# Optimization experiments

Hardware: AMD Instinct MI355X
Metric: run time of the kernel (lower is better)

The kernel has to match this reference:

```python
import jax, jax.numpy as jnp
import numpy as np


def setup_inputs() -> dict:
    key = jax.random.key(0)
    k1, k2 = jax.random.split(key)
    B, N, M = 8, 8192, 8192
    points1 = jax.random.normal(k1, (B, N, 2), dtype=jnp.float32)
    points2 = jax.random.normal(k2, (B, M, 2), dtype=jnp.float32)
    return {"points1": points1, "points2": points2}


def reference(points1, points2):
    # points1: [B, N, 2], points2: [B, M, 2]
    # Squared pairwise distances via |a|^2 + |b|^2 - 2 a.b  -> [B, N, M]
    p1_sq = jnp.sum(points1 * points1, axis=-1)  # [B, N]
    p2_sq = jnp.sum(points2 * points2, axis=-1)  # [B, M]
    cross = jnp.einsum("bnd,bmd->bnm", points1, points2)  # [B, N, M]
    sqdist = p1_sq[:, :, None] + p2_sq[:, None, :] - 2.0 * cross
    dist1 = jnp.min(sqdist, axis=2)  # [B, N]: NN of each p1 point in p2
    dist2 = jnp.min(sqdist, axis=1)  # [B, M]: NN of each p2 point in p1
    cost = jnp.mean(dist1, axis=-1) + jnp.mean(dist2, axis=-1)  # [B]
    return jnp.sum(cost)
```

## Files before the change

kernel.cpp:

```cpp
#include <hip/hip_runtime.h>


#define BATCH 8
#define NPTS  8192
#define TPB   256
#define IPT   16
#define PPB   (TPB * IPT)
#define TILES (NPTS / PPB)
#define S     32
#define JCH   (NPTS / S)
#define PARTN (2 * BATCH * S * NPTS)

__device__ inline float min3f(float a, float b, float c) {
    float d;
    asm("v_min3_f32 %0, %1, %2, %3" : "=v"(d) : "v"(a), "v"(b), "v"(c));
    return d;
}

__device__ inline float2 pkfma(float2 a, float2 b, float2 c) {
    float2 d;
    asm("v_pk_fma_f32 %0, %1, %2, %3" : "=v"(d) : "v"(a), "v"(b), "v"(c));
    return d;
}

__global__ __launch_bounds__(TPB, 4)
void chamfer_partial(const float* __restrict__ p1, const float* __restrict__ p2,
                     float* __restrict__ partial ) {
    __shared__ __align__(16) float qx[JCH];
    __shared__ __align__(16) float qy[JCH];
    __shared__ __align__(16) float qz[JCH];

    int blk   = blockIdx.x;
    int split = blk & (S - 1);      blk >>= 5;
    int tile  = blk & (TILES - 1);  blk >>= 1;
    int b     = blk & (BATCH - 1);  blk >>= 3;
    int dir   = blk;

    const float2* a  = (const float2*)(dir ? p2 : p1) + (size_t)b * NPTS;
    const float2* bp = (const float2*)(dir ? p1 : p2) + (size_t)b * NPTS + split * JCH;

    int t = threadIdx.x;

    {
        float2 v = bp[t];
        qx[t] = v.x;
        qy[t] = v.y;
        qz[t] = fmaf(v.x, v.x, v.y * v.y);
    }

    int pt_base = tile * PPB;
    float2 xp2[IPT], yp2[IPT];
    float  m[IPT];
#pragma unroll
    for (int k = 0; k < IPT; ++k) {
        float2 v = a[pt_base + k * TPB + t];
        xp2[k] = make_float2(-2.0f * v.x, -2.0f * v.x);
        yp2[k] = make_float2(-2.0f * v.y, -2.0f * v.y);
        m[k]   = 3.0e38f;
    }

    __syncthreads();

    for (int j = 0; j < JCH; j += 8) {
        float4 x03 = *(const float4*)&qx[j];
        float4 x47 = *(const float4*)&qx[j + 4];
        float4 y03 = *(const float4*)&qy[j];
        float4 y47 = *(const float4*)&qy[j + 4];
        float4 z03 = *(const float4*)&qz[j];
        float4 z47 = *(const float4*)&qz[j + 4];
        float2 x01 = make_float2(x03.x, x03.y), x23 = make_float2(x03.z, x03.w);
        float2 x45 = make_float2(x47.x, x47.y), x67 = make_float2(x47.z, x47.w);
        float2 y01 = make_float2(y03.x, y03.y), y23 = make_float2(y03.z, y03.w);
        float2 y45 = make_float2(y47.x, y47.y), y67 = make_float2(y47.z, y47.w);
        float2 z01 = make_float2(z03.x, z03.y), z23 = make_float2(z03.z, z03.w);
        float2 z45 = make_float2(z47.x, z47.y), z67 = make_float2(z47.z, z47.w);
#pragma unroll
        for (int k = 0; k < IPT; ++k) {
            float2 a01 = pkfma(yp2[k], y01, pkfma(xp2[k], x01, z01));
            float2 a23 = pkfma(yp2[k], y23, pkfma(xp2[k], x23, z23));
            float2 a45 = pkfma(yp2[k], y45, pkfma(xp2[k], x45, z45));
            float2 a67 = pkfma(yp2[k], y67, pkfma(xp2[k], x67, z67));
            m[k] = min3f(m[k], a01.x, a01.y);
            m[k] = min3f(m[k], a23.x, a23.y);
            m[k] = min3f(m[k], a45.x, a45.y);
            m[k] = min3f(m[k], a67.x, a67.y);
        }
    }

    float* outp = partial + ((size_t)((dir * BATCH + b) * S + split)) * NPTS + pt_base;
#pragma unroll
    for (int k = 0; k < IPT; ++k)
        outp[k * TPB + t] = m[k];
}

__global__ __launch_bounds__(TPB)
void chamfer_reduce(const float* __restrict__ p1, const float* __restrict__ p2,
                    const float* __restrict__ partial, float* __restrict__ bsum) {
    int gid   = blockIdx.x * TPB + threadIdx.x;
    int point = gid & (NPTS - 1);
    int rest  = gid >> 13;
    int b     = rest & (BATCH - 1);
    int dir   = rest >> 3;

    const float* base = partial + ((size_t)(dir * BATCH + b) * S) * NPTS + point;
    float m = base[0];
#pragma unroll
    for (int s = 1; s < S; ++s)
        m = fminf(m, base[(size_t)s * NPTS]);

    float2 v = ((const float2*)(dir ? p2 : p1))[(size_t)b * NPTS + point];
    float d = m + fmaf(v.x, v.x, v.y * v.y);

#pragma unroll
    for (int off = 32; off > 0; off >>= 1)
        d += __shfl_down(d, off, 64);

    __shared__ float wsum[TPB / 64];
    int lane = threadIdx.x & 63;
    int w    = threadIdx.x >> 6;
    if (lane == 0) wsum[w] = d;
    __syncthreads();
    if (threadIdx.x == 0)
        bsum[blockIdx.x] = wsum[0] + wsum[1] + wsum[2] + wsum[3];
}

__global__ __launch_bounds__(TPB)
void chamfer_final(const float* __restrict__ bsum, float* __restrict__ out) {
    int t = threadIdx.x;
    float s = bsum[t] + bsum[t + TPB];

#pragma unroll
    for (int off = 32; off > 0; off >>= 1)
        s += __shfl_down(s, off, 64);

    __shared__ float wsum[TPB / 64];
    int lane = t & 63;
    int w    = t >> 6;
    if (lane == 0) wsum[w] = s;
    __syncthreads();
    if (t == 0)
        *out = (wsum[0] + wsum[1] + wsum[2] + wsum[3]) * (1.0f / NPTS);
}

extern "C" void kernel_launch(void* const* d_in, const int* in_sizes, int n_in,
                              void* d_out, int out_size, void* d_ws, size_t ws_size,
                              hipStream_t stream) {
    const float* p1 = (const float*)d_in[0];
    const float* p2 = (const float*)d_in[1];
    float* out      = (float*)d_out;
    float* partial  = (float*)d_ws;
    float* bsum     = partial + PARTN;

    chamfer_partial<<<2 * BATCH * TILES * S, TPB, 0, stream>>>(p1, p2, partial);
    chamfer_reduce<<<2 * BATCH * NPTS / TPB, TPB, 0, stream>>>(p1, p2, partial, bsum);
    chamfer_final<<<1, TPB, 0, stream>>>(bsum, out);
}
```

Baseline: 119.4 us.

## Compute pairwise distances with bf16 split-precision MFMA instead of packed FP32 FMA

Adds a prep kernel that splits each coordinate and squared norm into hi/lo bf16 parts and packs them into MFMA fragment layouts. The full squared distance, including both norms, then comes from a single 16x16x32 bf16 MFMA per tile pair instead of packed FP32 FMAs. Row minima are reduced with lane shuffles, and the split count drops from 32 to 4, which shrinks the partial buffer. The risk is precision: the hi/lo bf16 products may not match FP32 closely enough. Extra costs are the prep pass and the zero-padded K slots, which waste MFMA work.

```diff
diff --git a/kernel.cpp b/kernel.cpp
--- a/kernel.cpp
+++ b/kernel.cpp
@@ -4,98 +4,139 @@
 #define BATCH 8
 #define NPTS  8192
 #define TPB   256
-#define IPT   16
-#define PPB   (TPB * IPT)
-#define TILES (NPTS / PPB)
-#define S     32
-#define JCH   (NPTS / S)
+#define S     4
 #define PARTN (2 * BATCH * S * NPTS)
+#define NPTOT (BATCH * NPTS)
+#define NTIL  (NPTOT / 16)
+#define TILB  (NPTS / 16)
+#define RBLKS (2 * BATCH * NPTS / TPB)
+#define GRIDP (2 * BATCH * 16 * S)
 
-__device__ inline float min3f(float a, float b, float c) {
-    float d;
-    asm("v_min3_f32 %0, %1, %2, %3" : "=v"(d) : "v"(a), "v"(b), "v"(c));
-    return d;
+typedef __attribute__((ext_vector_type(8))) short short8;
+typedef __attribute__((ext_vector_type(4))) float float4v;
+
+__device__ inline ushort bf16rne(float f) {
+    uint u = __float_as_uint(f);
+    u = u + 0x7FFFu + ((u >> 16) & 1u);
+    return (ushort)(u >> 16);
 }
+__device__ inline float bfloat(ushort h) { return __uint_as_float(((uint)h) << 16); }
 
-__device__ inline float2 pkfma(float2 a, float2 b, float2 c) {
-    float2 d;
-    asm("v_pk_fma_f32 %0, %1, %2, %3" : "=v"(d) : "v"(a), "v"(b), "v"(c));
-    return d;
+__global__ __launch_bounds__(TPB)
+void chamfer_prep(const float* __restrict__ p1, const float* __restrict__ p2,
+                  ushort* __restrict__ A1, ushort* __restrict__ B1,
+                  ushort* __restrict__ A2, ushort* __restrict__ B2) {
+    int idx   = blockIdx.x * TPB + threadIdx.x;
+    int which = idx >= NPTOT;
+    int p     = idx & (NPTOT - 1);
+    float2 v = ((const float2*)(which ? p2 : p1))[p];
+    float x = v.x, y = v.y;
+    float z = fmaf(x, x, y * y);
+    ushort xh = bf16rne(x); float xhf = bfloat(xh);
+    ushort xl = bf16rne(x - xhf);
+    ushort yh = bf16rne(y); float yhf = bfloat(yh);
+    ushort yl = bf16rne(y - yhf);
+    ushort zh = bf16rne(z); float zhf = bfloat(zh);
+    ushort zl = bf16rne(z - zhf);
+    const ushort one = 0x3F80;
+    int T = p >> 4, row = p & 15;
+    short8 zz = {0, 0, 0, 0, 0, 0, 0, 0};
+
+    ushort* Ab = (which ? A2 : A1) + (size_t)T * 512 + row * 8;
+    short8 ak0 = {(short)xh, (short)xh, (short)xl, (short)yh,
+                  (short)yh, (short)yl, (short)zh, (short)zl};
+    short8 ak1 = {(short)one, (short)one, 0, 0, 0, 0, 0, 0};
+    *(short8*)(Ab)       = ak0;
+    *(short8*)(Ab + 128) = ak1;
+    *(short8*)(Ab + 256) = zz;
+    *(short8*)(Ab + 384) = zz;
+
+    ushort m2xh = bf16rne(-2.0f * xhf), m2xl = bf16rne(-2.0f * bfloat(xl));
+    ushort m2yh = bf16rne(-2.0f * yhf), m2yl = bf16rne(-2.0f * bfloat(yl));
+    ushort* Bb = (which ? B2 : B1) + (size_t)T * 512 + row * 8;
+    short8 bk0 = {(short)m2xh, (short)m2xl, (short)m2xh, (short)m2yh,
+                  (short)m2yl, (short)m2yh, (short)one, (short)one};
+    short8 bk1 = {(short)zh, (short)zl, 0, 0, 0, 0, 0, 0};
+    *(short8*)(Bb)       = bk0;
+    *(short8*)(Bb + 128) = bk1;
+    *(short8*)(Bb + 256) = zz;
+    *(short8*)(Bb + 384) = zz;
 }
 
 __global__ __launch_bounds__(TPB, 4)
-void chamfer_partial(const float* __restrict__ p1, const float* __restrict__ p2,
+void chamfer_partial(const ushort* __restrict__ A1, const ushort* __restrict__ B1,
+                     const ushort* __restrict__ A2, const ushort* __restrict__ B2,
                      float* __restrict__ partial ) {
-    __shared__ __align__(16) float qx[JCH];
-    __shared__ __align__(16) float qy[JCH];
-    __shared__ __align__(16) float qz[JCH];
+    __shared__ float rows_lds[512];
 
-    int blk   = blockIdx.x;
-    int split = blk & (S - 1);      blk >>= 5;
-    int tile  = blk & (TILES - 1);  blk >>= 1;
-    int b     = blk & (BATCH - 1);  blk >>= 3;
-    int dir   = blk;
+    int bid  = blockIdx.x;
+    int jblk = bid & (S - 1);
+    int iblk = (bid >> 2) & 15;
+    int b    = (bid >> 6) & 7;
+    int dir  = bid >> 9;
 
-    const float2* a  = (const float2*)(dir ? p2 : p1) + (size_t)b * NPTS;
-    const float2* bp = (const float2*)(dir ? p1 : p2) + (size_t)b * NPTS + split * JCH;
+    const ushort* Ab = dir ? A2 : A1;
+    const ushort* Bb = dir ? B1 : B2;
 
-    int t = threadIdx.x;
+    int t = threadIdx.x, w = t >> 6, l = t & 63;
+    int lkc = l >> 4, lrow = l & 15;
+    size_t fo = (size_t)lkc * 128 + lrow * 8;
 
-    {
-        float2 v = bp[t];
-        qx[t] = v.x;
-        qy[t] = v.y;
-        qz[t] = fmaf(v.x, v.x, v.y * v.y);
-    }
+    short8 afr[8];
+    int TA = b * TILB + iblk * 32 + w * 8;
+#pragma unroll
+    for (int rt = 0; rt < 8; ++rt)
+        afr[rt] = *(const short8*)(Ab + (size_t)(TA + rt) * 512 + fo);
 
-    int pt_base = tile * PPB;
-    float2 xp2[IPT], yp2[IPT];
-    float  m[IPT];
+    float rowmin[8][4];
 #pragma unroll
-    for (int k = 0; k < IPT; ++k) {
-        float2 v = a[pt_base + k * TPB + t];
-        xp2[k] = make_float2(-2.0f * v.x, -2.0f * v.x);
-        yp2[k] = make_float2(-2.0f * v.y, -2.0f * v.y);
-        m[k]   = 3.0e38f;
-    }
+    for (int rt = 0; rt < 8; ++rt)
+#pragma unroll
+        for (int r = 0; r < 4; ++r) rowmin[rt][r] = 3.0e38f;
 
-    __syncthreads();
+    int TB = b * TILB + jblk * 128;
+    const float4v zero = {0.0f, 0.0f, 0.0f, 0.0f};
 
-    for (int j = 0; j < JCH; j += 8) {
-        float4 x03 = *(const float4*)&qx[j];
-        float4 x47 = *(const float4*)&qx[j + 4];
-        float4 y03 = *(const float4*)&qy[j];
-        float4 y47 = *(const float4*)&qy[j + 4];
-        float4 z03 = *(const float4*)&qz[j];
-        float4 z47 = *(const float4*)&qz[j + 4];
-        float2 x01 = make_float2(x03.x, x03.y), x23 = make_float2(x03.z, x03.w);
-        float2 x45 = make_float2(x47.x, x47.y), x67 = make_float2(x47.z, x47.w);
-        float2 y01 = make_float2(y03.x, y03.y), y23 = make_float2(y03.z, y03.w);
-        float2 y45 = make_float2(y47.x, y47.y), y67 = make_float2(y47.z, y47.w);
-        float2 z01 = make_float2(z03.x, z03.y), z23 = make_float2(z03.z, z03.w);
-        float2 z45 = make_float2(z47.x, z47.y), z67 = make_float2(z47.z, z47.w);
+    for (int ct = 0; ct < 128; ++ct) {
+        short8 bf = *(const short8*)(Bb + (size_t)(TB + ct) * 512 + fo);
 #pragma unroll
-        for (int k = 0; k < IPT; ++k) {
-            float2 a01 = pkfma(yp2[k], y01, pkfma(xp2[k], x01, z01));
-            float2 a23 = pkfma(yp2[k], y23, pkfma(xp2[k], x23, z23));
-            float2 a45 = pkfma(yp2[k], y45, pkfma(xp2[k], x45, z45));
-            float2 a67 = pkfma(yp2[k], y67, pkfma(xp2[k], x67, z67));
-            m[k] = min3f(m[k], a01.x, a01.y);
-            m[k] = min3f(m[k], a23.x, a23.y);
-            m[k] = min3f(m[k], a45.x, a45.y);
-            m[k] = min3f(m[k], a67.x, a67.y);
+        for (int rt = 0; rt < 8; ++rt) {
+            float4v c = __builtin_amdgcn_mfma_f32_16x16x32_bf16(afr[rt], bf, zero, 0, 0, 0);
+            rowmin[rt][0] = fminf(rowmin[rt][0], c[0]);
+            rowmin[rt][1] = fminf(rowmin[rt][1], c[1]);
+            rowmin[rt][2] = fminf(rowmin[rt][2], c[2]);
+            rowmin[rt][3] = fminf(rowmin[rt][3], c[3]);
         }
     }
 
-    float* outp = partial + ((size_t)((dir * BATCH + b) * S + split)) * NPTS + pt_base;
 #pragma unroll
-    for (int k = 0; k < IPT; ++k)
-        outp[k * TPB + t] = m[k];
+    for (int rt = 0; rt < 8; ++rt)
+#pragma unroll
+        for (int r = 0; r < 4; ++r) {
+            float mm = rowmin[rt][r];
+            mm = fminf(mm, __shfl_xor(mm, 1, 64));
+            mm = fminf(mm, __shfl_xor(mm, 2, 64));
+            mm = fminf(mm, __shfl_xor(mm, 4, 64));
+            mm = fminf(mm, __shfl_xor(mm, 8, 64));
+            rowmin[rt][r] = mm;
+        }
+
+    if (lrow == 0) {
+#pragma unroll
+        for (int rt = 0; rt < 8; ++rt)
+#pragma unroll
+            for (int r = 0; r < 4; ++r)
+                rows_lds[w * 128 + rt * 16 + lkc * 4 + r] = rowmin[rt][r];
+    }
+    __syncthreads();
+
+    float* op = partial + ((size_t)((dir * BATCH + b) * S + jblk)) * NPTS + iblk * 512;
+    op[t]       = rows_lds[t];
+    op[t + 256] = rows_lds[t + 256];
 }
 
 __global__ __launch_bounds__(TPB)
-void chamfer_reduce(const float* __restrict__ p1, const float* __restrict__ p2,
-                    const float* __restrict__ partial, float* __restrict__ bsum) {
+void chamfer_reduce(const float* __restrict__ partial, float* __restrict__ bsum) {
     int gid   = blockIdx.x * TPB + threadIdx.x;
     int point = gid & (NPTS - 1);
     int rest  = gid >> 13;
@@ -103,13 +144,10 @@
     int dir   = rest >> 3;
 
     const float* base = partial + ((size_t)(dir * BATCH + b) * S) * NPTS + point;
-    float m = base[0];
+    float d = base[0];
 #pragma unroll
     for (int s = 1; s < S; ++s)
-        m = fminf(m, base[(size_t)s * NPTS]);
-
-    float2 v = ((const float2*)(dir ? p2 : p1))[(size_t)b * NPTS + point];
-    float d = m + fmaf(v.x, v.x, v.y * v.y);
+        d = fminf(d, base[(size_t)s * NPTS]);
 
 #pragma unroll
     for (int off = 32; off > 0; off >>= 1)
@@ -128,11 +166,9 @@
 void chamfer_final(const float* __restrict__ bsum, float* __restrict__ out) {
     int t = threadIdx.x;
     float s = bsum[t] + bsum[t + TPB];
-
 #pragma unroll
     for (int off = 32; off > 0; off >>= 1)
         s += __shfl_down(s, off, 64);
-
     __shared__ float wsum[TPB / 64];
     int lane = t & 63;
     int w    = t >> 6;
@@ -150,8 +186,13 @@
     float* out      = (float*)d_out;
     float* partial  = (float*)d_ws;
     float* bsum     = partial + PARTN;
+    ushort* A1      = (ushort*)(bsum + 512);
+    ushort* B1      = A1 + (size_t)NTIL * 512;
+    ushort* A2      = B1 + (size_t)NTIL * 512;
+    ushort* B2      = A2 + (size_t)NTIL * 512;
 
-    chamfer_partial<<<2 * BATCH * TILES * S, TPB, 0, stream>>>(p1, p2, partial);
-    chamfer_reduce<<<2 * BATCH * NPTS / TPB, TPB, 0, stream>>>(p1, p2, partial, bsum);
+    chamfer_prep<<<2 * NPTOT / TPB, TPB, 0, stream>>>(p1, p2, A1, B1, A2, B2);
+    chamfer_partial<<<GRIDP, TPB, 0, stream>>>(A1, B1, A2, B2, partial);
+    chamfer_reduce<<<RBLKS, TPB, 0, stream>>>(partial, bsum);
     chamfer_final<<<1, TPB, 0, stream>>>(bsum, out);
 }
```

Result: slower. 190.9 us (+59.8%).
